# Optimization experiments

Hardware: AMD Instinct MI355X
Metric: run time of the kernel (lower is better)

Reference implementation:

```python
import jax, jax.numpy as jnp
import numpy as np

CHANNELS = 512
GROUPS = 32
EPS = 1e-6


def setup_inputs() -> dict:
    key = jax.random.key(0)
    ks = jax.random.split(key, 10)
    C = CHANNELS
    s = 1.0 / np.sqrt(C)
    return {
        "hidden_states": jax.random.normal(ks[0], (4, 64, 64, C), dtype=jnp.float32),
        "gn_scale": jnp.ones((C,), dtype=jnp.float32),
        "gn_bias": jnp.zeros((C,), dtype=jnp.float32),
        "wq": jax.random.normal(ks[1], (C, C), dtype=jnp.float32) * s,
        "bq": jnp.zeros((C,), dtype=jnp.float32),
        "wk": jax.random.normal(ks[2], (C, C), dtype=jnp.float32) * s,
        "bk": jnp.zeros((C,), dtype=jnp.float32),
        "wv": jax.random.normal(ks[3], (C, C), dtype=jnp.float32) * s,
        "bv": jnp.zeros((C,), dtype=jnp.float32),
        "wo": jax.random.normal(ks[4], (C, C), dtype=jnp.float32) * s,
        "bo": jnp.zeros((C,), dtype=jnp.float32),
    }


def reference(hidden_states, gn_scale, gn_bias, wq, bq, wk, bk, wv, bv, wo, bo):
    B, H, W, C = hidden_states.shape
    residual = hidden_states
    L = H * W
    x = hidden_states.reshape(B, L, C)

    # GroupNorm: stats over (spatial, channels-within-group), per batch per group
    xg = x.reshape(B, L, GROUPS, C // GROUPS)
    mean = jnp.mean(xg, axis=(1, 3), keepdims=True)
    var = jnp.var(xg, axis=(1, 3), keepdims=True)
    xn = ((xg - mean) * jax.lax.rsqrt(var + EPS)).reshape(B, L, C)
    xn = xn * gn_scale + gn_bias

    # QKV projections (heads=1, head_dim=C)
    q = xn @ wq + bq
    k = xn @ wk + bk
    v = xn @ wv + bv

    scale = 1.0 / jnp.sqrt(jnp.asarray(C, dtype=q.dtype))
    scores = jnp.einsum('bld,bsd->bls', q, k) * scale  # [B, L, L]
    attn = jax.nn.softmax(scores, axis=-1)
    out = jnp.einsum('bls,bsd->bld', attn, v)

    out = out @ wo + bo
    return out.reshape(B, H, W, C) + residual
```

## Files before the change

kernel.cpp:

```cpp
#include <hip/hip_runtime.h>
#include <hip/hip_bf16.h>
#include <stdint.h>

#define BATCH 4
#define SEQ   4096
#define CH    512
#define NGRP  32
#define GEPS  1e-6f

typedef short  short8  __attribute__((ext_vector_type(8)));
typedef float  floatx4 __attribute__((ext_vector_type(4)));
typedef long   longx2  __attribute__((ext_vector_type(2)));

static __device__ __forceinline__ short bf16b(float f) {
    __hip_bfloat16 h = __float2bfloat16(f);
    return __builtin_bit_cast(short, h);
}
static __device__ __forceinline__ float bf2f(short s) {
    unsigned u = ((unsigned)(unsigned short)s) << 16;
    return __builtin_bit_cast(float, u);
}
static __device__ __forceinline__ char fp8b(float f) {
    int pk = __builtin_amdgcn_cvt_pk_fp8_f32(f, f, 0, false);
    return (char)(pk & 0xff);
}

static __device__ __forceinline__ void dma16(const void* g, void* l) {
    __builtin_amdgcn_global_load_lds(
        (const __attribute__((address_space(1))) unsigned int*)g,
        (__attribute__((address_space(3))) unsigned int*)l, 16, 0, 0);
}

static __device__ __forceinline__ float rowmax16(float x) {
    int xi = __builtin_bit_cast(int, x);
    x = fmaxf(x, __builtin_bit_cast(float, __builtin_amdgcn_update_dpp(xi, xi, 0x128, 0xf, 0xf, true)));
    xi = __builtin_bit_cast(int, x);
    x = fmaxf(x, __builtin_bit_cast(float, __builtin_amdgcn_update_dpp(xi, xi, 0x124, 0xf, 0xf, true)));
    xi = __builtin_bit_cast(int, x);
    x = fmaxf(x, __builtin_bit_cast(float, __builtin_amdgcn_update_dpp(xi, xi, 0x122, 0xf, 0xf, true)));
    xi = __builtin_bit_cast(int, x);
    x = fmaxf(x, __builtin_bit_cast(float, __builtin_amdgcn_update_dpp(xi, xi, 0x121, 0xf, 0xf, true)));
    return x;
}

__global__ __launch_bounds__(256) void gn_partial_kernel(const float* __restrict__ x,
                                                         float* __restrict__ statsraw) {
    int blk = blockIdx.x;
    int t = threadIdx.x;
    size_t row0 = (size_t)blk * 64;
    int qd = t & 127;
    int rh = t >> 7;
    const float* base = x + row0 * 512 + qd * 4;
    float s1 = 0.f, s2 = 0.f;
    #pragma unroll 4
    for (int i = 0; i < 32; ++i) {
        int r = rh + i * 2;
        float4 v = *reinterpret_cast<const float4*>(base + (size_t)r * 512);
        s1 += v.x + v.y + v.z + v.w;
        s2 += v.x * v.x + v.y * v.y + v.z * v.z + v.w * v.w;
    }
    __shared__ float a1[256], a2[256];
    a1[t] = s1; a2[t] = s2;
    __syncthreads();
    if (t < 32) {
        float u1 = 0.f, u2 = 0.f;
        #pragma unroll
        for (int e = 0; e < 4; ++e) {
            u1 += a1[t * 4 + e] + a1[128 + t * 4 + e];
            u2 += a2[t * 4 + e] + a2[128 + t * 4 + e];
        }
        int b = (int)(row0 >> 12);
        atomicAdd(&statsraw[(b * 32 + t) * 2],     u1);
        atomicAdd(&statsraw[(b * 32 + t) * 2 + 1], u2);
    }
}

__global__ __launch_bounds__(256) void gn_apply_kernel(const float* __restrict__ x,
                                                       const float* __restrict__ statsraw,
                                                       const float* __restrict__ gsc,
                                                       const float* __restrict__ gbs,
                                                       short* __restrict__ xn) {
    int i4 = blockIdx.x * 256 + threadIdx.x;
    int base = i4 * 4;
    int b = base >> 21;
    int c = base & 511;
    int sidx = (b * 32 + (c >> 4)) * 2;
    float s1 = statsraw[sidx], s2 = statsraw[sidx + 1];
    float mean = s1 * (1.f / 65536.f);
    float var  = s2 * (1.f / 65536.f) - mean * mean;
    float rstd = rsqrtf(var + GEPS);
    float4 xv = reinterpret_cast<const float4*>(x)[i4];
    float4 sv = *reinterpret_cast<const float4*>(gsc + c);
    float4 bv = *reinterpret_cast<const float4*>(gbs + c);
    union { short s[4]; uint2 u; } p;
    p.s[0] = bf16b((xv.x - mean) * rstd * sv.x + bv.x);
    p.s[1] = bf16b((xv.y - mean) * rstd * sv.y + bv.y);
    p.s[2] = bf16b((xv.z - mean) * rstd * sv.z + bv.z);
    p.s[3] = bf16b((xv.w - mean) * rstd * sv.w + bv.w);
    reinterpret_cast<uint2*>(xn)[i4] = p.u;
}

__global__ __launch_bounds__(256) void wtrans_kernel(const float* __restrict__ w0,
                                                     const float* __restrict__ w1,
                                                     const float* __restrict__ w2,
                                                     const float* __restrict__ w3,
                                                     short* __restrict__ wT) {
    const float* w = (blockIdx.z == 0) ? w0 : (blockIdx.z == 1) ? w1
                   : (blockIdx.z == 2) ? w2 : w3;
    short* out = wT + (size_t)blockIdx.z * CH * CH;
    int n0 = blockIdx.x * 32, k0 = blockIdx.y * 32;
    int tx = threadIdx.x, ty = threadIdx.y;
    __shared__ float s[32][33];
    #pragma unroll
    for (int i = 0; i < 4; ++i) {
        int kk = ty + i * 8;
        s[kk][tx] = w[(size_t)(k0 + kk) * CH + n0 + tx];
    }
    __syncthreads();
    #pragma unroll
    for (int i = 0; i < 4; ++i) {
        int nn = ty + i * 8;
        out[(size_t)(n0 + nn) * CH + k0 + tx] = bf16b(s[tx][nn]);
    }
}

__global__ __launch_bounds__(256) void gemm_qkv_kernel(const short* __restrict__ A,
                                                       const short* __restrict__ wT,
                                                       const float* __restrict__ bq,
                                                       const float* __restrict__ bk,
                                                       const float* __restrict__ bv,
                                                       char* __restrict__ q8,
                                                       char* __restrict__ k8,
                                                       char* __restrict__ vT8) {
    __shared__ short As[128 * 64];
    __shared__ short Bs[128 * 64];
    __shared__ char  vls[128 * 144];
    int m0 = blockIdx.x * 128;
    int nblk = blockIdx.y;
    int which = nblk >> 2;
    int n0 = (nblk & 3) * 128;
    const short* BT = wT + (size_t)which * 512 * 512;
    const float* bias = (which == 0) ? bq : (which == 1) ? bk : bv;
    int t = threadIdx.x;
    int w = t >> 6, lane = t & 63;
    int wr = w >> 1, wc = w & 1;
    int l15 = lane & 15, l4 = lane >> 4;
    floatx4 acc[4][4];
    #pragma unroll
    for (int i = 0; i < 4; ++i)
        #pragma unroll
        for (int j = 0; j < 4; ++j) acc[i][j] = (floatx4){0.f, 0.f, 0.f, 0.f};

    for (int k0 = 0; k0 < 512; k0 += 64) {
        __syncthreads();
        #pragma unroll
        for (int i = 0; i < 4; ++i) {
            int c = i * 256 + t;
            int row = c >> 3, j = (c & 7) ^ (row & 7);
            dma16(&A[(size_t)(m0 + row) * 512 + k0 + j * 8], &As[(c & ~63) * 8]);
            dma16(&BT[(size_t)(n0 + row) * 512 + k0 + j * 8], &Bs[(c & ~63) * 8]);
        }
        __syncthreads();
        #pragma unroll
        for (int kk = 0; kk < 64; kk += 32) {
            short8 af[4], bf[4];
            #pragma unroll
            for (int i = 0; i < 4; ++i) {
                int row = wr * 64 + i * 16 + l15;
                int j = (kk >> 3) + l4;
                af[i] = *reinterpret_cast<const short8*>(&As[(row * 8 + (j ^ (l15 & 7))) * 8]);
            }
            #pragma unroll
            for (int j2 = 0; j2 < 4; ++j2) {
                int row = wc * 64 + j2 * 16 + l15;
                int j = (kk >> 3) + l4;
                bf[j2] = *reinterpret_cast<const short8*>(&Bs[(row * 8 + (j ^ (l15 & 7))) * 8]);
            }
            #pragma unroll
            for (int i = 0; i < 4; ++i)
                #pragma unroll
                for (int j2 = 0; j2 < 4; ++j2)
                    acc[i][j2] = __builtin_amdgcn_mfma_f32_16x16x32_bf16(af[i], bf[j2], acc[i][j2], 0, 0, 0);
        }
    }
    if (which == 0) {
        #pragma unroll
        for (int i = 0; i < 4; ++i)
            #pragma unroll
            for (int j = 0; j < 4; ++j)
                #pragma unroll
                for (int r = 0; r < 4; ++r) {
                    int row = m0 + wr * 64 + i * 16 + l4 * 4 + r;
                    int col = n0 + wc * 64 + j * 16 + l15;
                    q8[(size_t)row * 512 + col] = fp8b(acc[i][j][r] + bias[col]);
                }
    } else if (which == 1) {
        #pragma unroll
        for (int i = 0; i < 4; ++i)
            #pragma unroll
            for (int j = 0; j < 4; ++j)
                #pragma unroll
                for (int r = 0; r < 4; ++r) {
                    int row = m0 + wr * 64 + i * 16 + l4 * 4 + r;
                    int col = n0 + wc * 64 + j * 16 + l15;
                    int bb = row >> 12, s = row & 4095;
                    size_t idx = (size_t)bb * 2097152 + (size_t)(s >> 5) * 16384
                               + (s & 15) * 1024 + ((s >> 4) & 1) * 8
                               + (col >> 3) * 16 + (col & 7);
                    k8[idx] = fp8b(acc[i][j][r] + bias[col]);
                }
    } else {
        __syncthreads();
        #pragma unroll
        for (int i = 0; i < 4; ++i)
            #pragma unroll
            for (int j = 0; j < 4; ++j)
                #pragma unroll
                for (int r = 0; r < 4; ++r) {
                    int rl = wr * 64 + i * 16 + l4 * 4 + r;
                    int rp = (rl & ~31) | (((rl & 15) << 1) | ((rl >> 4) & 1));
                    int cl = wc * 64 + j * 16 + l15;
                    vls[cl * 144 + rp] = fp8b(acc[i][j][r] + bias[n0 + cl]);
                }
        __syncthreads();
        int b = m0 >> 12, l0 = m0 & 4095;
        #pragma unroll
        for (int p = 0; p < 4; ++p) {
            int slot = p * 256 + t;
            int c = slot >> 3, off = (slot & 7) * 16;
            uint4 v;
            __builtin_memcpy(&v, &vls[c * 144 + off], 16);
            int dcol = n0 + c;
            int g = dcol >> 5, rr = dcol & 15, h = (dcol >> 4) & 1;
            int s = l0 + off;
            int sb = s >> 5, mb = (s & 31) >> 3;
            char* dst = vT8 + (size_t)b * 2097152 + (size_t)sb * 16384
                      + (size_t)((((g * 16 + rr) * 4 + mb) * 16) + h * 8);
            unsigned long long lo = ((unsigned long long)v.y << 32) | v.x;
            unsigned long long hi = ((unsigned long long)v.w << 32) | v.z;
            *reinterpret_cast<unsigned long long*>(dst)      = lo;
            *reinterpret_cast<unsigned long long*>(dst + 16) = hi;
        }
    }
}

__global__ __launch_bounds__(256) void gemm_bt_kernel(const short* __restrict__ Opart,
                                                      const float* __restrict__ ml,
                                                      const short* __restrict__ BT,
                                                      const float* __restrict__ bias,
                                                      float* __restrict__ outf,
                                                      const float* __restrict__ resid) {
    __shared__ short As[128 * 64];
    __shared__ short Bs[128 * 64];
    int m0 = blockIdx.x * 128, n0 = blockIdx.y * 128;
    int t = threadIdx.x;
    int w = t >> 6, lane = t & 63;
    int wr = w >> 1, wc = w & 1;
    int l15 = lane & 15, l4 = lane >> 4;
    const size_t PART = (size_t)BATCH * SEQ;
    floatx4 acc[4][4];
    #pragma unroll
    for (int i = 0; i < 4; ++i)
        #pragma unroll
        for (int j = 0; j < 4; ++j) acc[i][j] = (floatx4){0.f, 0.f, 0.f, 0.f};

    for (int k0 = 0; k0 < 512; k0 += 64) {
        __syncthreads();
        #pragma unroll
        for (int i = 0; i < 4; ++i) {
            int c = i * 256 + t;
            int rl = c >> 3, j = (c & 7) ^ (rl & 7);
            size_t rowg = (size_t)(m0 + rl);
            const short* s0 = Opart + rowg * 512 + k0 + j * 8;
            const short* s1 = s0 + PART * 512;
            uint4 a0 = *reinterpret_cast<const uint4*>(s0);
            uint4 a1 = *reinterpret_cast<const uint4*>(s1);
            float mA = ml[rowg * 2],          lA = ml[rowg * 2 + 1];
            float mB = ml[(PART + rowg) * 2], lB = ml[(PART + rowg) * 2 + 1];
            float mm = fmaxf(mA, mB);
            float e0 = exp2f(mA - mm), e1 = exp2f(mB - mm);
            float inv = 1.f / (e0 * lA + e1 * lB);
            e0 *= inv; e1 *= inv;
            union { uint4 u; short s[8]; } ua, ub, uo;
            ua.u = a0; ub.u = a1;
            #pragma unroll
            for (int e = 0; e < 8; ++e)
                uo.s[e] = bf16b(bf2f(ua.s[e]) * e0 + bf2f(ub.s[e]) * e1);
            *reinterpret_cast<uint4*>(&As[c * 8]) = uo.u;
            dma16(&BT[(size_t)(n0 + rl) * 512 + k0 + j * 8], &Bs[(c & ~63) * 8]);
        }
        __syncthreads();
        #pragma unroll
        for (int kk = 0; kk < 64; kk += 32) {
            short8 af[4], bf[4];
            #pragma unroll
            for (int i = 0; i < 4; ++i) {
                int row = wr * 64 + i * 16 + l15;
                int j = (kk >> 3) + l4;
                af[i] = *reinterpret_cast<const short8*>(&As[(row * 8 + (j ^ (l15 & 7))) * 8]);
            }
            #pragma unroll
            for (int j2 = 0; j2 < 4; ++j2) {
                int row = wc * 64 + j2 * 16 + l15;
                int j = (kk >> 3) + l4;
                bf[j2] = *reinterpret_cast<const short8*>(&Bs[(row * 8 + (j ^ (l15 & 7))) * 8]);
            }
            #pragma unroll
            for (int i = 0; i < 4; ++i)
                #pragma unroll
                for (int j2 = 0; j2 < 4; ++j2)
                    acc[i][j2] = __builtin_amdgcn_mfma_f32_16x16x32_bf16(af[i], bf[j2], acc[i][j2], 0, 0, 0);
        }
    }
    #pragma unroll
    for (int i = 0; i < 4; ++i)
        #pragma unroll
        for (int j = 0; j < 4; ++j)
            #pragma unroll
            for (int r = 0; r < 4; ++r) {
                int row = m0 + wr * 64 + i * 16 + l4 * 4 + r;
                int col = n0 + wc * 64 + j * 16 + l15;
                float vv = acc[i][j][r] + bias[col];
                outf[(size_t)row * 512 + col] = vv + resid[(size_t)row * 512 + col];
            }
}

__global__ __launch_bounds__(256, 2) void flash_kernel(const char* __restrict__ q8,
                                                       const char* __restrict__ k8,
                                                       const char* __restrict__ v8,
                                                       short* __restrict__ Opart,
                                                       float* __restrict__ ml) {
    __shared__ __align__(16) char smem[68096];
    int bx = blockIdx.x;
    int pb = bx & 7;
    int part = pb >> 2, b = pb & 3;
    int q0 = (bx >> 3) * 64;
    int t = threadIdx.x, w = t >> 6, lane = t & 63;
    int l15 = lane & 15, l4 = lane >> 4;
    const float c2 = 0.06375873735f;
    const float MARGIN = 7.2134752f;

    long qf[16];
    {
        const char* qrow = q8 + ((size_t)b * SEQ + q0 + w * 16 + l15) * 512;
        #pragma unroll
        for (int ks = 0; ks < 16; ++ks)
            qf[ks] = *reinterpret_cast<const long*>(qrow + ks * 32 + l4 * 8);
    }

    floatx4 acc[32];
    #pragma unroll
    for (int i = 0; i < 32; ++i) acc[i] = (floatx4){0.f, 0.f, 0.f, 0.f};
    floatx4 lacc = (floatx4){0.f, 0.f, 0.f, 0.f};
    float mused[4] = {-1e30f, -1e30f, -1e30f, -1e30f};

    const long ones = 0x3838383838383838L;

    const char* kbase = k8 + (size_t)b * SEQ * 512;
    const char* vbase = v8 + (size_t)b * 512 * SEQ;
    const int sb0 = part * 64;

    const int ksw = l15 & 7;
    const int vsw = (l15 >> 1) & 3;
    const char* kA_E = smem + ((l15 * 64 + (l4 ^ ksw)) << 4);
    const char* kA_O = smem + ((l15 * 64 + ((4 + l4) ^ ksw)) << 4);
    const char* vA   = smem + 32768 + ((l15 * 4 + (l4 ^ vsw)) << 4);
    char* Ps = smem + 65536 + w * 640;

    int kSrc[4], vSrc[4];
    #pragma unroll
    for (int i = 0; i < 4; ++i) {
        int c = i * 256 + t;
        kSrc[i] = (((c & ~63) | ((c & 63) ^ ((c >> 6) & 7))) << 4);
        vSrc[i] = (((c & ~3)  | ((c & 3)  ^ ((c >> 3) & 3))) << 4);
    }
    const int ldsD = (t & ~63) << 4;

    auto stage = [&](int sb, int buf) {
        const char* kt = kbase + (size_t)sb * 16384;
        const char* vt = vbase + (size_t)sb * 16384;
        char* Kd = smem + buf * 16384 + ldsD;
        char* Vd = smem + 32768 + buf * 16384 + ldsD;
        #pragma unroll
        for (int i = 0; i < 4; ++i) dma16(kt + kSrc[i], Kd + i * 4096);
        #pragma unroll
        for (int i = 0; i < 4; ++i) dma16(vt + vSrc[i], Vd + i * 4096);
    };

    stage(sb0, 0);
    __syncthreads();

    for (int it = 0; it < 64; ++it) {
        int cur = it & 1;
        int coff = cur << 14;
        if (it + 1 < 64) stage(sb0 + it + 1, 1 - cur);

        floatx4 sa0 = (floatx4){0.f, 0.f, 0.f, 0.f};
        floatx4 sa1 = (floatx4){0.f, 0.f, 0.f, 0.f};
        __builtin_amdgcn_s_setprio(1);
        #pragma unroll
        for (int j = 0; j < 8; ++j) {
            longx2 kE = *reinterpret_cast<const longx2*>(kA_E + coff + j * 128);
            longx2 kO = *reinterpret_cast<const longx2*>(kA_O + coff + j * 128);
            sa0 = __builtin_amdgcn_mfma_f32_16x16x32_fp8_fp8(qf[2 * j],     kE[0], sa0, 0, 0, 0);
            sa1 = __builtin_amdgcn_mfma_f32_16x16x32_fp8_fp8(qf[2 * j],     kE[1], sa1, 0, 0, 0);
            sa0 = __builtin_amdgcn_mfma_f32_16x16x32_fp8_fp8(qf[2 * j + 1], kO[0], sa0, 0, 0, 0);
            sa1 = __builtin_amdgcn_mfma_f32_16x16x32_fp8_fp8(qf[2 * j + 1], kO[1], sa1, 0, 0, 0);
        }
        __builtin_amdgcn_s_setprio(0);

        float v0[4], v1[4], nm4[4];
        bool need = false;
        #pragma unroll
        for (int r = 0; r < 4; ++r) {
            v0[r] = sa0[r] * c2; v1[r] = sa1[r] * c2;
            nm4[r] = rowmax16(fmaxf(v0[r], v1[r]));
            need |= (nm4[r] > mused[r] + MARGIN);
        }
        if (__ballot(need)) {
            #pragma unroll
            for (int r = 0; r < 4; ++r) {
                float nm = fmaxf(mused[r], nm4[r]);
                float al = exp2f(mused[r] - nm);
                lacc[r] *= al;
                #pragma unroll
                for (int i = 0; i < 32; ++i) acc[i][r] *= al;
                mused[r] = nm;
            }
        }
        #pragma unroll
        for (int r = 0; r < 4; ++r) {
            int pk = __builtin_amdgcn_cvt_pk_fp8_f32(exp2f(v0[r] - mused[r]),
                                                     exp2f(v1[r] - mused[r]), 0, false);
            *reinterpret_cast<short*>(Ps + (l4 * 4 + r) * 40 + l15 * 2) = (short)pk;
        }

        long pf;
        __builtin_memcpy(&pf, (const char*)__builtin_assume_aligned(Ps + l15 * 40 + l4 * 8, 8), 8);
        __builtin_amdgcn_s_setprio(1);
        lacc = __builtin_amdgcn_mfma_f32_16x16x32_fp8_fp8(pf, ones, lacc, 0, 0, 0);
        #pragma unroll
        for (int g = 0; g < 16; ++g) {
            longx2 vv = *reinterpret_cast<const longx2*>(vA + coff + g * 1024);
            acc[2 * g]     = __builtin_amdgcn_mfma_f32_16x16x32_fp8_fp8(pf, vv[0], acc[2 * g],     0, 0, 0);
            acc[2 * g + 1] = __builtin_amdgcn_mfma_f32_16x16x32_fp8_fp8(pf, vv[1], acc[2 * g + 1], 0, 0, 0);
        }
        __builtin_amdgcn_s_setprio(0);

        __syncthreads();
    }

    short* obase = Opart + (((size_t)part * BATCH + b) * SEQ + q0 + w * 16) * 512;
    #pragma unroll
    for (int r = 0; r < 4; ++r) {
        #pragma unroll
        for (int tt = 0; tt < 32; ++tt)
            obase[(size_t)(l4 * 4 + r) * 512 + tt * 16 + l15] = bf16b(acc[tt][r]);
    }
    if (l15 == 0) {
        #pragma unroll
        for (int r = 0; r < 4; ++r) {
            size_t rowg = ((size_t)part * BATCH + b) * SEQ + q0 + w * 16 + l4 * 4 + r;
            ml[rowg * 2]     = mused[r];
            ml[rowg * 2 + 1] = lacc[r];
        }
    }
}

extern "C" void kernel_launch(void* const* d_in, const int* in_sizes, int n_in,
                              void* d_out, int out_size, void* d_ws, size_t ws_size,
                              hipStream_t stream) {
    const float* x   = (const float*)d_in[0];
    const float* gsc = (const float*)d_in[1];
    const float* gbs = (const float*)d_in[2];
    const float* wq  = (const float*)d_in[3];
    const float* bq  = (const float*)d_in[4];
    const float* wk  = (const float*)d_in[5];
    const float* bk  = (const float*)d_in[6];
    const float* wv  = (const float*)d_in[7];
    const float* bv  = (const float*)d_in[8];
    const float* wo  = (const float*)d_in[9];
    const float* bo  = (const float*)d_in[10];
    float* out = (float*)d_out;

    char* ws = (char*)d_ws;
    const size_t MB = 1ull << 20;
    short* xn    = (short*)ws;
    char*  q8    = (char*)(ws + 16 * MB);
    char*  k8    = (char*)(ws + 24 * MB);
    char*  vT8   = (char*)(ws + 32 * MB);
    short* Opart = (short*)(ws + 40 * MB);
    short* wT    = (short*)(ws + 72 * MB);
    float* stats = (float*)(ws + 74 * MB);
    float* ml    = (float*)(ws + 74 * MB + 65536);

    hipMemsetAsync(stats, 0, 256 * sizeof(float), stream);
    gn_partial_kernel<<<256, 256, 0, stream>>>(x, stats);
    gn_apply_kernel<<<8192, 256, 0, stream>>>(x, stats, gsc, gbs, xn);
    wtrans_kernel<<<dim3(16, 16, 4), dim3(32, 8), 0, stream>>>(wq, wk, wv, wo, wT);

    short* woT = wT + 786432;

    gemm_qkv_kernel<<<dim3(128, 12), 256, 0, stream>>>(xn, wT, bq, bk, bv, q8, k8, vT8);
    flash_kernel<<<512, 256, 0, stream>>>(q8, k8, vT8, Opart, ml);
    gemm_bt_kernel<<<dim3(128, 4), 256, 0, stream>>>(Opart, ml, woT, bo, out, x);
}
```

Baseline: 292.9 us.

## Split PV output columns across waves, sharing P tiles through LDS

The P·V stage is repartitioned. Each wave now owns a 128-column slice of the output for all 64 query rows, instead of all 512 columns for its own 16 rows. Each wave publishes its fp8 P tile, rescale factors and a rescale flag to LDS, and after a barrier every wave reads all four P tiles. V fragments are loaded once per wave and reused across the four P tiles, which cuts V LDS traffic per wave. In exchange it adds an extra __syncthreads per iteration, extra LDS reads for P and alpha, and removes the s_setprio hints.

```diff
diff --git a/kernel.cpp b/kernel.cpp
--- a/kernel.cpp
+++ b/kernel.cpp
@@ -330,7 +330,7 @@
                                                        const char* __restrict__ v8,
                                                        short* __restrict__ Opart,
                                                        float* __restrict__ ml) {
-    __shared__ __align__(16) char smem[68096];
+    __shared__ __align__(16) char smem[68368];
     int bx = blockIdx.x;
     int pb = bx & 7;
     int part = pb >> 2, b = pb & 3;
@@ -364,8 +364,11 @@
     const int vsw = (l15 >> 1) & 3;
     const char* kA_E = smem + ((l15 * 64 + (l4 ^ ksw)) << 4);
     const char* kA_O = smem + ((l15 * 64 + ((4 + l4) ^ ksw)) << 4);
-    const char* vA   = smem + 32768 + ((l15 * 4 + (l4 ^ vsw)) << 4);
-    char* Ps = smem + 65536 + w * 640;
+    const char* vA   = smem + 32768 + w * 4096 + ((l15 * 4 + (l4 ^ vsw)) << 4);
+    char* Ps  = smem + 65536 + w * 640;
+    char* Pb  = smem + 65536;
+    char* alB = smem + 68096;
+    int*  flg = (int*)(smem + 68352);
 
     int kSrc[4], vSrc[4];
     #pragma unroll
@@ -397,7 +400,6 @@
 
         floatx4 sa0 = (floatx4){0.f, 0.f, 0.f, 0.f};
         floatx4 sa1 = (floatx4){0.f, 0.f, 0.f, 0.f};
-        __builtin_amdgcn_s_setprio(1);
         #pragma unroll
         for (int j = 0; j < 8; ++j) {
             longx2 kE = *reinterpret_cast<const longx2*>(kA_E + coff + j * 128);
@@ -407,7 +409,6 @@
             sa0 = __builtin_amdgcn_mfma_f32_16x16x32_fp8_fp8(qf[2 * j + 1], kO[0], sa0, 0, 0, 0);
             sa1 = __builtin_amdgcn_mfma_f32_16x16x32_fp8_fp8(qf[2 * j + 1], kO[1], sa1, 0, 0, 0);
         }
-        __builtin_amdgcn_s_setprio(0);
 
         float v0[4], v1[4], nm4[4];
         bool need = false;
@@ -417,46 +418,75 @@
             nm4[r] = rowmax16(fmaxf(v0[r], v1[r]));
             need |= (nm4[r] > mused[r] + MARGIN);
         }
-        if (__ballot(need)) {
+        floatx4 alv = (floatx4){1.f, 1.f, 1.f, 1.f};
+        int myf = (__ballot(need) != 0ull) ? 1 : 0;
+        if (myf) {
             #pragma unroll
             for (int r = 0; r < 4; ++r) {
                 float nm = fmaxf(mused[r], nm4[r]);
                 float al = exp2f(mused[r] - nm);
                 lacc[r] *= al;
-                #pragma unroll
-                for (int i = 0; i < 32; ++i) acc[i][r] *= al;
                 mused[r] = nm;
-            }
-        }
+                alv[r] = al;
+            }
+        }
+        if (l15 == 0) *reinterpret_cast<floatx4*>(alB + w * 64 + l4 * 16) = alv;
+        if (lane == 0) flg[w] = myf;
         #pragma unroll
         for (int r = 0; r < 4; ++r) {
             int pk = __builtin_amdgcn_cvt_pk_fp8_f32(exp2f(v0[r] - mused[r]),
                                                      exp2f(v1[r] - mused[r]), 0, false);
             *reinterpret_cast<short*>(Ps + (l4 * 4 + r) * 40 + l15 * 2) = (short)pk;
         }
-
-        long pf;
-        __builtin_memcpy(&pf, (const char*)__builtin_assume_aligned(Ps + l15 * 40 + l4 * 8, 8), 8);
-        __builtin_amdgcn_s_setprio(1);
-        lacc = __builtin_amdgcn_mfma_f32_16x16x32_fp8_fp8(pf, ones, lacc, 0, 0, 0);
-        #pragma unroll
-        for (int g = 0; g < 16; ++g) {
-            longx2 vv = *reinterpret_cast<const longx2*>(vA + coff + g * 1024);
-            acc[2 * g]     = __builtin_amdgcn_mfma_f32_16x16x32_fp8_fp8(pf, vv[0], acc[2 * g],     0, 0, 0);
-            acc[2 * g + 1] = __builtin_amdgcn_mfma_f32_16x16x32_fp8_fp8(pf, vv[1], acc[2 * g + 1], 0, 0, 0);
-        }
-        __builtin_amdgcn_s_setprio(0);
-
-        __syncthreads();
-    }
-
-    short* obase = Opart + (((size_t)part * BATCH + b) * SEQ + q0 + w * 16) * 512;
-    #pragma unroll
-    for (int r = 0; r < 4; ++r) {
-        #pragma unroll
-        for (int tt = 0; tt < 32; ++tt)
-            obase[(size_t)(l4 * 4 + r) * 512 + tt * 16 + l15] = bf16b(acc[tt][r]);
-    }
+        {
+            long pfOwn;
+            __builtin_memcpy(&pfOwn, (const char*)__builtin_assume_aligned(Ps + l15 * 40 + l4 * 8, 8), 8);
+            lacc = __builtin_amdgcn_mfma_f32_16x16x32_fp8_fp8(pfOwn, ones, lacc, 0, 0, 0);
+        }
+
+        __syncthreads();
+
+        int anyf = flg[0] | flg[1] | flg[2] | flg[3];
+        long pfA[4];
+        #pragma unroll
+        for (int c = 0; c < 4; ++c)
+            __builtin_memcpy(&pfA[c], (const char*)__builtin_assume_aligned(
+                                 Pb + c * 640 + l15 * 40 + l4 * 8, 8), 8);
+        longx2 vv0 = *reinterpret_cast<const longx2*>(vA + coff);
+        longx2 vv1 = *reinterpret_cast<const longx2*>(vA + coff + 1024);
+        longx2 vv2 = *reinterpret_cast<const longx2*>(vA + coff + 2048);
+        longx2 vv3 = *reinterpret_cast<const longx2*>(vA + coff + 3072);
+        if (anyf) {
+            #pragma unroll
+            for (int c = 0; c < 4; ++c) {
+                floatx4 a = *reinterpret_cast<const floatx4*>(alB + c * 64 + l4 * 16);
+                #pragma unroll
+                for (int dt = 0; dt < 8; ++dt) acc[c * 8 + dt] *= a;
+            }
+        }
+        #pragma unroll
+        for (int c = 0; c < 4; ++c) {
+            acc[c*8+0] = __builtin_amdgcn_mfma_f32_16x16x32_fp8_fp8(pfA[c], vv0[0], acc[c*8+0], 0, 0, 0);
+            acc[c*8+1] = __builtin_amdgcn_mfma_f32_16x16x32_fp8_fp8(pfA[c], vv0[1], acc[c*8+1], 0, 0, 0);
+            acc[c*8+2] = __builtin_amdgcn_mfma_f32_16x16x32_fp8_fp8(pfA[c], vv1[0], acc[c*8+2], 0, 0, 0);
+            acc[c*8+3] = __builtin_amdgcn_mfma_f32_16x16x32_fp8_fp8(pfA[c], vv1[1], acc[c*8+3], 0, 0, 0);
+            acc[c*8+4] = __builtin_amdgcn_mfma_f32_16x16x32_fp8_fp8(pfA[c], vv2[0], acc[c*8+4], 0, 0, 0);
+            acc[c*8+5] = __builtin_amdgcn_mfma_f32_16x16x32_fp8_fp8(pfA[c], vv2[1], acc[c*8+5], 0, 0, 0);
+            acc[c*8+6] = __builtin_amdgcn_mfma_f32_16x16x32_fp8_fp8(pfA[c], vv3[0], acc[c*8+6], 0, 0, 0);
+            acc[c*8+7] = __builtin_amdgcn_mfma_f32_16x16x32_fp8_fp8(pfA[c], vv3[1], acc[c*8+7], 0, 0, 0);
+        }
+
+        __syncthreads();
+    }
+
+    short* obase = Opart + (((size_t)part * BATCH + b) * SEQ + q0) * 512 + w * 128;
+    #pragma unroll
+    for (int c = 0; c < 4; ++c)
+        #pragma unroll
+        for (int dt = 0; dt < 8; ++dt)
+            #pragma unroll
+            for (int r = 0; r < 4; ++r)
+                obase[(size_t)(c * 16 + l4 * 4 + r) * 512 + dt * 16 + l15] = bf16b(acc[c * 8 + dt][r]);
     if (l15 == 0) {
         #pragma unroll
         for (int r = 0; r < 4; ++r) {
```

Measured after the change: 296.3 us. No clear change (+1.2%).
